# Kernel tuning notes

Measured on AMD Instinct MI355X. Metric: run time of the kernel, lower is better.

## Reference

```python
import jax, jax.numpy as jnp
import numpy as np

B, T, C, H, W = 2, 8, 256, 24, 24
NH = 8
HC = C // NH          # 32 head channels
KT, KHW = 3, 9        # offset conv kernel
ST, SHW = 2, 8        # offset conv stride
EPS = 1e-5


def _p(key, shape):
    return jax.random.normal(key, shape, dtype=jnp.float32) * 0.05


def setup_inputs() -> dict:
    ks = jax.random.split(jax.random.key(0), 16)
    return {
        "x": jax.random.normal(ks[0], (B, T, C, H, W), dtype=jnp.float32),
        "w_in": _p(ks[1], (C, C)), "b_in": _p(ks[2], (C,)),
        "w_q": _p(ks[3], (C, C)), "b_q": _p(ks[4], (C,)),
        "w_off_dw": _p(ks[5], (HC, 1, KT, KHW, KHW)), "b_off_dw": _p(ks[6], (HC,)),
        "ln_g": jnp.ones((HC,), jnp.float32), "ln_b": jnp.zeros((HC,), jnp.float32),
        "w_off_proj": _p(ks[7], (3, HC)),
        "w_k": _p(ks[8], (C, C)), "b_k": _p(ks[9], (C,)),
        "w_v": _p(ks[10], (C, C)), "b_v": _p(ks[11], (C,)),
        "rpe_w1": _p(ks[12], (32, 3)), "rpe_b1": _p(ks[13], (32,)),
        "rpe_w2": _p(ks[14], (1, 32)),
    }


def _conv1x1(x, w, b):
    # x: (B,C,T,H,W), w: (Co,Ci) -> pointwise Conv3d
    return jnp.einsum('bcthw,oc->bothw', x, w) + b[None, :, None, None, None]


def _trilinear(img, gx, gy, gz):
    # torch F.grid_sample(mode='bilinear', align_corners=True) for 5D input.
    # img: (G,Ch,T,H,W); gx->W axis, gy->H axis, gz->T axis, coords in [-1,1], shape (G,S)
    G, Ch, Td, Hd, Wd = img.shape
    ix = (gx + 1.0) * 0.5 * (Wd - 1)
    iy = (gy + 1.0) * 0.5 * (Hd - 1)
    iz = (gz + 1.0) * 0.5 * (Td - 1)
    x0 = jnp.floor(ix); y0 = jnp.floor(iy); z0 = jnp.floor(iz)
    fx = ix - x0; fy = iy - y0; fz = iz - z0
    x0i = jnp.clip(x0.astype(jnp.int32), 0, Wd - 1); x1i = jnp.clip(x0i + 1, 0, Wd - 1)
    y0i = jnp.clip(y0.astype(jnp.int32), 0, Hd - 1); y1i = jnp.clip(y0i + 1, 0, Hd - 1)
    z0i = jnp.clip(z0.astype(jnp.int32), 0, Td - 1); z1i = jnp.clip(z0i + 1, 0, Td - 1)
    bidx = jnp.arange(G)[:, None]

    def g(zi, yi, xi):
        return img[bidx, :, zi, yi, xi]  # (G,S,Ch)

    wz0, wz1 = (1.0 - fz)[..., None], fz[..., None]
    wy0, wy1 = (1.0 - fy)[..., None], fy[..., None]
    wx0, wx1 = (1.0 - fx)[..., None], fx[..., None]
    return (g(z0i, y0i, x0i) * wz0 * wy0 * wx0 + g(z0i, y0i, x1i) * wz0 * wy0 * wx1 +
            g(z0i, y1i, x0i) * wz0 * wy1 * wx0 + g(z0i, y1i, x1i) * wz0 * wy1 * wx1 +
            g(z1i, y0i, x0i) * wz1 * wy0 * wx0 + g(z1i, y0i, x1i) * wz1 * wy0 * wx1 +
            g(z1i, y1i, x0i) * wz1 * wy1 * wx0 + g(z1i, y1i, x1i) * wz1 * wy1 * wx1)


def reference(x, w_in, b_in, w_q, b_q, w_off_dw, b_off_dw, ln_g, ln_b, w_off_proj,
              w_k, b_k, w_v, b_v, rpe_w1, rpe_b1, rpe_w2):
    scale = HC ** (-0.5)
    xc = _conv1x1(jnp.transpose(x, (0, 2, 1, 3, 4)), w_in, b_in)       # (B,C,T,H,W)
    q = _conv1x1(xc, w_q, b_q)
    q_off = q.reshape(B * NH, HC, T, H, W)
    # depthwise offset conv: kernel (3,9,9), stride (2,8,8), pad (1,4,4)
    off = jax.lax.conv_general_dilated(
        q_off, w_off_dw, (ST, SHW, SHW),
        ((KT // 2, KT // 2), (KHW // 2, KHW // 2), (KHW // 2, KHW // 2)),
        dimension_numbers=('NCDHW', 'OIDHW', 'NCDHW'), feature_group_count=HC)
    off = off + b_off_dw[None, :, None, None, None]
    Tk, Hk, Wk = off.shape[2], off.shape[3], off.shape[4]
    o = jnp.transpose(off, (0, 2, 3, 4, 1))                             # (G,Tk,Hk,Wk,HC)
    mu = o.mean(-1, keepdims=True)
    var = ((o - mu) ** 2).mean(-1, keepdims=True)
    o = (o - mu) / jnp.sqrt(var + EPS) * ln_g + ln_b
    o = jax.nn.gelu(o, approximate=False)
    offset = jnp.einsum('bthwc,pc->bthwp', o, w_off_proj)               # (G,Tk,Hk,Wk,3)
    # reference points (linspace(0.5, K-0.5, K) normalized by (K-1))
    rt = ((jnp.arange(Tk, dtype=jnp.float32) + 0.5) / (Tk - 1.0)) * 2.0 - 1.0
    ry = ((jnp.arange(Hk, dtype=jnp.float32) + 0.5) / (Hk - 1.0)) * 2.0 - 1.0
    rx = ((jnp.arange(Wk, dtype=jnp.float32) + 0.5) / (Wk - 1.0)) * 2.0 - 1.0
    ref = jnp.stack(jnp.meshgrid(rt, ry, rx, indexing='ij'), axis=-1)   # (Tk,Hk,Wk,3)
    pos = jnp.clip(offset + ref, -1.0, 1.0)                             # offset_range_factor < 0 path
    G = B * NH
    n = Tk * Hk * Wk
    m = T * H * W
    posf = pos.reshape(G, n, 3)                                         # (t, y, x)
    # torch passes grid = pos[..., (0,2,1)] -> grid (x_w, y_h, z_t) = (pos_t, pos_x, pos_y)
    xs = _trilinear(xc.reshape(G, HC, T, H, W), posf[..., 0], posf[..., 2], posf[..., 1])  # (G,n,HC)
    x_sampled = jnp.transpose(xs, (0, 2, 1)).reshape(B, C, Tk, Hk, Wk)
    k = _conv1x1(x_sampled, w_k, b_k).reshape(G, HC, n)
    v = _conv1x1(x_sampled, w_v, b_v).reshape(G, HC, n)
    qf = q.reshape(G, HC, m)
    attn = jnp.einsum('bcm,bcn->bmn', qf, k) * scale                    # (G,m,n)
    # log-CPB bias (source normalizes y by W-1 and x by H-1; faithful)
    qt = (jnp.arange(T, dtype=jnp.float32) / (T - 1.0)) * 2.0 - 1.0
    qy = (jnp.arange(H, dtype=jnp.float32) / (W - 1.0)) * 2.0 - 1.0
    qx = (jnp.arange(W, dtype=jnp.float32) / (H - 1.0)) * 2.0 - 1.0
    qg = jnp.stack(jnp.meshgrid(qt, qy, qx, indexing='ij'), axis=-1).reshape(m, 3)
    disp = (qg[None, :, None, :] - posf[:, None, :, :]) * 4.0           # (G,m,n,3)
    disp = jnp.sign(disp) * jnp.log2(jnp.abs(disp) + 1.0) / 3.0         # log2(8) = 3
    hbias = jax.nn.relu(jnp.einsum('gmnp,hp->gmnh', disp, rpe_w1) + rpe_b1)
    attn = attn + jnp.einsum('gmnh,oh->gmno', hbias, rpe_w2)[..., 0]
    attn = jax.nn.softmax(attn, axis=2)
    out = jnp.einsum('bmn,bcn->bcm', attn, v).reshape(B, C, T, H, W)
    return jnp.transpose(out, (0, 2, 1, 3, 4))                          # (B,T,C,H,W)
```

## Files before the change

kernel.cpp:

```cpp
#include <hip/hip_runtime.h>
#include <hip/hip_bf16.h>

typedef unsigned short ushortT;
typedef __attribute__((ext_vector_type(8))) short bf16x8;
typedef __attribute__((ext_vector_type(4))) float f32x4;

#define WS_XC   0
#define WS_QB   2359296
#define WS_POS  3538944
#define WS_K    3540736
#define WS_V    3559168
#define WS_WC   3577600
#define WS_B512 3675904
#define WS_FLAG 3676416
#define WS_XHI  3677184
#define WS_XLO  4856832
#define WS_WHI  6036480
#define WS_WLO  6102016

__device__ __forceinline__ float bf2f(ushortT u) {
  union { unsigned int i; float f; } c; c.i = ((unsigned int)u) << 16; return c.f;
}
__device__ __forceinline__ ushortT f2bf(float f) {
  union { float f; unsigned int i; } c; c.f = f;
  unsigned int lsb = (c.i >> 16) & 1;
  return (ushortT)((c.i + 0x7fff + lsb) >> 16);
}
__device__ __forceinline__ float ldg_f(const void* p, int i, int bf) {
  return bf ? bf2f(((const ushortT*)p)[i]) : ((const float*)p)[i];
}

__global__ void k_detect(const void* x, int* flagout) {
  int lane = threadIdx.x;
  const ushortT* u = (const ushortT*)x;
  int wild = 0;
  for (int i = lane; i < 512; i += 64) {
    ushortT s = u[i];
    int e = (s >> 7) & 0xFF;
    if (e != 0 && (e < 90 || e > 160)) wild++;
  }
  for (int off = 32; off; off >>= 1) wild += __shfl_down(wild, off);
  if (lane == 0) flagout[0] = (wild > 40) ? 0 : 1;
}

__global__ __launch_bounds__(256) void k_wc(const void* w_in, const void* b_in, const void* w_q,
                                            const void* b_q, float* wc, float* bias512, const int* flag) {
  int o = blockIdx.x, tid = threadIdx.x, bf = flag[0];
  __shared__ float wq_s[256];
  __shared__ float red[256];
  wq_s[tid] = ldg_f(w_q, o * 256 + tid, bf);
  __syncthreads();
  float s = 0.f;
#pragma unroll 8
  for (int j = 0; j < 256; j++) s += wq_s[j] * ldg_f(w_in, j * 256 + tid, bf);
  wc[o * 256 + tid] = s;
  red[tid] = wq_s[tid] * ldg_f(b_in, tid, bf);
  __syncthreads();
  for (int m = 128; m; m >>= 1) {
    if (tid < m) red[tid] += red[tid + m];
    __syncthreads();
  }
  if (tid == 0) bias512[256 + o] = red[0] + ldg_f(b_q, o, bf);
  if (o == 0) bias512[tid] = ldg_f(b_in, tid, bf);
}

__global__ __launch_bounds__(256) void k_xsplit(const void* x, ushortT* xhi, ushortT* xlo,
                                                const int* flag) {
  int bf = flag[0];
  int i0 = (blockIdx.x * 256 + threadIdx.x) * 4;
  float v[4];
  if (bf) {
    ushort4 u = *(const ushort4*)((const ushortT*)x + i0);
    v[0] = bf2f(u.x); v[1] = bf2f(u.y); v[2] = bf2f(u.z); v[3] = bf2f(u.w);
  } else {
    float4 f = *(const float4*)((const float*)x + i0);
    v[0] = f.x; v[1] = f.y; v[2] = f.z; v[3] = f.w;
  }
  ushortT hi[4], lo[4];
#pragma unroll
  for (int j = 0; j < 4; j++) {
    hi[j] = f2bf(v[j]);
    lo[j] = f2bf(v[j] - bf2f(hi[j]));
  }
  *(ushort4*)(xhi + i0) = make_ushort4(hi[0], hi[1], hi[2], hi[3]);
  *(ushort4*)(xlo + i0) = make_ushort4(lo[0], lo[1], lo[2], lo[3]);
}

__global__ __launch_bounds__(256) void k_wsplit(const void* w_in, const float* wc,
                                                ushortT* whi, ushortT* wlo, const int* flag) {
  int o = blockIdx.x, k = threadIdx.x, bf = flag[0];
  float v = (o < 256) ? ldg_f(w_in, o * 256 + k, bf) : wc[(o - 256) * 256 + k];
  ushortT h = f2bf(v);
  whi[o * 256 + k] = h;
  wlo[o * 256 + k] = f2bf(v - bf2f(h));
}

__global__ __launch_bounds__(256) void k_gemm_mfma(const ushortT* xhi, const ushortT* xlo,
                                                   const ushortT* whi, const ushortT* wlo,
                                                   const float* bias512, float* xc, ushortT* qb) {
  __shared__ ushortT Ah[64 * 40], Al[64 * 40];
  __shared__ ushortT Bh[64 * 40], Bl[64 * 40];
  int tid = threadIdx.x;
  int bid = blockIdx.x;
  int colT = bid / 144, rowT = bid % 144;
  int col0 = colT * 64;
  int row0 = rowT * 64;
  int bt = row0 / 576;
  int hw0 = row0 % 576;
  const int isW = (col0 < 256);
  int ar = tid & 63, aoct = tid >> 6;
  int bn = tid >> 2, bko = tid & 3;
  const ushortT* bsrcH = whi + (col0 + bn) * 256;
  const ushortT* bsrcL = wlo + (col0 + bn) * 256;
  int w = tid >> 6, l = tid & 63;
  int wr = w >> 1, wcq = w & 1;
  int lr = l & 15, lk = l >> 4;
  f32x4 acc[2][2] = {};

  for (int kt = 0; kt < 8; kt++) {
    {
      int kbase = (bt * 256 + kt * 32 + aoct * 8) * 576 + hw0 + ar;
      unsigned int h[8], lo[8];
#pragma unroll
      for (int j = 0; j < 8; j++) {
        h[j]  = xhi[kbase + j * 576];
        lo[j] = xlo[kbase + j * 576];
      }
      int4 ph, pl;
      ph.x = (int)(h[0] | (h[1] << 16));   ph.y = (int)(h[2] | (h[3] << 16));
      ph.z = (int)(h[4] | (h[5] << 16));   ph.w = (int)(h[6] | (h[7] << 16));
      pl.x = (int)(lo[0] | (lo[1] << 16)); pl.y = (int)(lo[2] | (lo[3] << 16));
      pl.z = (int)(lo[4] | (lo[5] << 16)); pl.w = (int)(lo[6] | (lo[7] << 16));
      *(int4*)&Ah[ar * 40 + aoct * 8] = ph;
      *(int4*)&Al[ar * 40 + aoct * 8] = pl;
    }
    {
      int4 vh = *(const int4*)(bsrcH + kt * 32 + bko * 8);
      int4 vl = *(const int4*)(bsrcL + kt * 32 + bko * 8);
      *(int4*)&Bh[bn * 40 + bko * 8] = vh;
      *(int4*)&Bl[bn * 40 + bko * 8] = vl;
    }
    __syncthreads();
    bf16x8 a0h = *(const bf16x8*)&Ah[(wr * 32 + 0 * 16 + lr) * 40 + lk * 8];
    bf16x8 a1h = *(const bf16x8*)&Ah[(wr * 32 + 1 * 16 + lr) * 40 + lk * 8];
    bf16x8 a0l = *(const bf16x8*)&Al[(wr * 32 + 0 * 16 + lr) * 40 + lk * 8];
    bf16x8 a1l = *(const bf16x8*)&Al[(wr * 32 + 1 * 16 + lr) * 40 + lk * 8];
    bf16x8 b0h = *(const bf16x8*)&Bh[(wcq * 32 + 0 * 16 + lr) * 40 + lk * 8];
    bf16x8 b1h = *(const bf16x8*)&Bh[(wcq * 32 + 1 * 16 + lr) * 40 + lk * 8];
    bf16x8 b0l = *(const bf16x8*)&Bl[(wcq * 32 + 0 * 16 + lr) * 40 + lk * 8];
    bf16x8 b1l = *(const bf16x8*)&Bl[(wcq * 32 + 1 * 16 + lr) * 40 + lk * 8];
    acc[0][0] = __builtin_amdgcn_mfma_f32_16x16x32_bf16(a0h, b0h, acc[0][0], 0, 0, 0);
    acc[0][0] = __builtin_amdgcn_mfma_f32_16x16x32_bf16(a0h, b0l, acc[0][0], 0, 0, 0);
    acc[0][0] = __builtin_amdgcn_mfma_f32_16x16x32_bf16(a0l, b0h, acc[0][0], 0, 0, 0);
    acc[0][1] = __builtin_amdgcn_mfma_f32_16x16x32_bf16(a0h, b1h, acc[0][1], 0, 0, 0);
    acc[0][1] = __builtin_amdgcn_mfma_f32_16x16x32_bf16(a0h, b1l, acc[0][1], 0, 0, 0);
    acc[0][1] = __builtin_amdgcn_mfma_f32_16x16x32_bf16(a0l, b1h, acc[0][1], 0, 0, 0);
    acc[1][0] = __builtin_amdgcn_mfma_f32_16x16x32_bf16(a1h, b0h, acc[1][0], 0, 0, 0);
    acc[1][0] = __builtin_amdgcn_mfma_f32_16x16x32_bf16(a1h, b0l, acc[1][0], 0, 0, 0);
    acc[1][0] = __builtin_amdgcn_mfma_f32_16x16x32_bf16(a1l, b0h, acc[1][0], 0, 0, 0);
    acc[1][1] = __builtin_amdgcn_mfma_f32_16x16x32_bf16(a1h, b1h, acc[1][1], 0, 0, 0);
    acc[1][1] = __builtin_amdgcn_mfma_f32_16x16x32_bf16(a1h, b1l, acc[1][1], 0, 0, 0);
    acc[1][1] = __builtin_amdgcn_mfma_f32_16x16x32_bf16(a1l, b1h, acc[1][1], 0, 0, 0);
    __syncthreads();
  }
#pragma unroll
  for (int m = 0; m < 2; m++) {
#pragma unroll
    for (int n = 0; n < 2; n++) {
#pragma unroll
      for (int i = 0; i < 4; i++) {
        int row = row0 + wr * 32 + m * 16 + lk * 4 + i;
        int col = col0 + wcq * 32 + n * 16 + lr;
        float v = acc[m][n][i] + bias512[col];
        if (isW) xc[row * 256 + col] = v;
        else     qb[row * 256 + (col - 256)] = f2bf(v);
      }
    }
  }
}

__global__ __launch_bounds__(256) void k_offsets(const ushortT* qb, const void* w_dw, const void* b_dw,
                                                 const void* ln_g, const void* ln_b, const void* w_proj,
                                                 float* pos, const int* flag) {
  __shared__ float wdw[243 * 33];
  __shared__ float part[8][33];
  int bid = blockIdx.x;
  int g = bid / 36, nn = bid % 36;
  int b = g >> 3, nh = g & 7;
  int tk = nn / 9, hk = (nn / 3) % 3, wk = nn % 3;
  int tid = threadIdx.x;
  int ch = tid & 31, grp = tid >> 5;
  int bf = flag[0];
  for (int i = tid; i < 7776; i += 256) {
    int c = i / 243, tap = i % 243;
    wdw[tap * 33 + c] = ldg_f(w_dw, i, bf);
  }
  __syncthreads();
  float sum = 0.f;
  for (int tap = grp; tap < 243; tap += 8) {
    int dt = tap / 81, rem = tap % 81, dh = rem / 9, dw = rem % 9;
    int t = tk * 2 - 1 + dt, h = hk * 8 - 4 + dh, w = wk * 8 - 4 + dw;
    if (t < 0 || t >= 8 || h < 0 || h >= 24 || w < 0 || w >= 24) continue;
    float qv = bf2f(qb[((b * 8 + t) * 576 + h * 24 + w) * 256 + nh * 32 + ch]);
    sum += qv * wdw[tap * 33 + ch];
  }
  part[grp][ch] = sum;
  __syncthreads();
  if (tid < 32) {
    float v = ldg_f(b_dw, ch, bf);
#pragma unroll
    for (int j = 0; j < 8; j++) v += part[j][ch];
    float s1 = v;
    for (int m = 16; m; m >>= 1) s1 += __shfl_xor(s1, m);
    float mu = s1 * (1.f / 32.f);
    float d = v - mu;
    float s2 = d * d;
    for (int m = 16; m; m >>= 1) s2 += __shfl_xor(s2, m);
    float o = d * rsqrtf(s2 * (1.f / 32.f) + 1e-5f) * ldg_f(ln_g, ch, bf) + ldg_f(ln_b, ch, bf);
    o = 0.5f * o * (1.f + erff(o * 0.70710678118654752f));
    float res[3];
#pragma unroll
    for (int p = 0; p < 3; p++) {
      float t3 = o * ldg_f(w_proj, p * 32 + ch, bf);
      for (int m = 16; m; m >>= 1) t3 += __shfl_xor(t3, m);
      res[p] = t3;
    }
    if (ch == 0) {
      float ref0 = ((tk + 0.5f) / 3.f) * 2.f - 1.f;
      float ref1 = ((hk + 0.5f) / 2.f) * 2.f - 1.f;
      float ref2 = ((wk + 0.5f) / 2.f) * 2.f - 1.f;
      pos[bid * 3 + 0] = fminf(1.f, fmaxf(-1.f, res[0] + ref0));
      pos[bid * 3 + 1] = fminf(1.f, fmaxf(-1.f, res[1] + ref1));
      pos[bid * 3 + 2] = fminf(1.f, fmaxf(-1.f, res[2] + ref2));
    }
  }
}

__global__ __launch_bounds__(256) void k_svkv(const float* xc_rm, const float* pos,
                                              const void* w_k, const void* b_k,
                                              const void* w_v, const void* b_v,
                                              float* k_rm, float* v_rm, const int* flag) {
  int bx = blockIdx.x;
  int sel = bx & 1, row = bx >> 1;
  int b = row / 36, nn = row % 36;
  int tid = threadIdx.x;
  int bf = flag[0];
  __shared__ float a[256];
  {
    int nh = tid >> 5;
    int g = b * 8 + nh;
    float p0 = pos[(g * 36 + nn) * 3 + 0];
    float p1 = pos[(g * 36 + nn) * 3 + 1];
    float p2 = pos[(g * 36 + nn) * 3 + 2];
    float ix = (p0 + 1.f) * 0.5f * 23.f;
    float iy = (p2 + 1.f) * 0.5f * 23.f;
    float iz = (p1 + 1.f) * 0.5f * 7.f;
    float x0f = floorf(ix), y0f = floorf(iy), z0f = floorf(iz);
    float fx = ix - x0f, fy = iy - y0f, fz = iz - z0f;
    int x0 = min(max((int)x0f, 0), 23), x1 = min(x0 + 1, 23);
    int y0 = min(max((int)y0f, 0), 23), y1 = min(y0 + 1, 23);
    int z0 = min(max((int)z0f, 0), 7),  z1 = min(z0 + 1, 7);
#define AT(z, y, x) xc_rm[(((b * 8 + (z)) * 576 + (y) * 24 + (x)) * 256 + tid)]
    a[tid] =
      AT(z0, y0, x0) * (1.f - fz) * (1.f - fy) * (1.f - fx) + AT(z0, y0, x1) * (1.f - fz) * (1.f - fy) * fx +
      AT(z0, y1, x0) * (1.f - fz) * fy * (1.f - fx)         + AT(z0, y1, x1) * (1.f - fz) * fy * fx +
      AT(z1, y0, x0) * fz * (1.f - fy) * (1.f - fx)         + AT(z1, y0, x1) * fz * (1.f - fy) * fx +
      AT(z1, y1, x0) * fz * fy * (1.f - fx)                 + AT(z1, y1, x1) * fz * fy * fx;
#undef AT
  }
  __syncthreads();
  const void* w = sel ? w_v : w_k;
  const void* bb = sel ? b_v : b_k;
  float s = 0.f;
  if (bf) {
    const ushortT* wp = (const ushortT*)w + tid * 256;
#pragma unroll 4
    for (int c = 0; c < 256; c += 8) {
      ushort4 k0 = *(const ushort4*)(wp + c), k1 = *(const ushort4*)(wp + c + 4);
      s += a[c+0]*bf2f(k0.x) + a[c+1]*bf2f(k0.y) + a[c+2]*bf2f(k0.z) + a[c+3]*bf2f(k0.w)
         + a[c+4]*bf2f(k1.x) + a[c+5]*bf2f(k1.y) + a[c+6]*bf2f(k1.z) + a[c+7]*bf2f(k1.w);
    }
  } else {
    const float* wp = (const float*)w + tid * 256;
#pragma unroll 4
    for (int c = 0; c < 256; c += 4) {
      float4 k4 = *(const float4*)(wp + c);
      s += a[c]*k4.x + a[c+1]*k4.y + a[c+2]*k4.z + a[c+3]*k4.w;
    }
  }
  float* outp = sel ? v_rm : k_rm;
  outp[row * 256 + tid] = s + ldg_f(bb, tid, bf);
}

__global__ __launch_bounds__(256) void k_attn(const ushortT* qb, const float* k_rm, const float* v_rm,
                                              const float* pos, const void* rpe_w1, const void* rpe_b1,
                                              const void* rpe_w2, void* outp, const int* flag) {
  __shared__ float ks[36][32];
  __shared__ float vs[36][32];
  __shared__ float poss[36][4];
  __shared__ float4 wab[32];
  __shared__ float w2s[32];
  int g = blockIdx.y, b = g >> 3, nh = g & 7;
  int tid = threadIdx.x;
  int bf = flag[0];
  for (int e = tid; e < 36 * 32; e += 256) {
    int nn = e >> 5, ch = e & 31;
    ks[nn][ch] = k_rm[(b * 36 + nn) * 256 + nh * 32 + ch];
    vs[nn][ch] = v_rm[(b * 36 + nn) * 256 + nh * 32 + ch];
  }
  if (tid < 32) {
    wab[tid] = make_float4(ldg_f(rpe_w1, tid * 3 + 0, bf), ldg_f(rpe_w1, tid * 3 + 1, bf),
                           ldg_f(rpe_w1, tid * 3 + 2, bf), ldg_f(rpe_b1, tid, bf));
    w2s[tid] = ldg_f(rpe_w2, tid, bf);
  }
  if (tid < 108) poss[tid / 3][tid % 3] = pos[g * 108 + tid];
  __syncthreads();

  int mm = blockIdx.x * 256 + tid;
  int t = mm / 576, hw = mm % 576, hh = hw / 24, wwi = hw % 24;
  float qreg[32];
  const ushort4* qp = (const ushort4*)&qb[(b * 4608 + mm) * 256 + nh * 32];
#pragma unroll
  for (int i = 0; i < 8; i++) {
    ushort4 u = qp[i];
    qreg[i * 4 + 0] = bf2f(u.x); qreg[i * 4 + 1] = bf2f(u.y);
    qreg[i * 4 + 2] = bf2f(u.z); qreg[i * 4 + 3] = bf2f(u.w);
  }
  float qg0 = t * (2.f / 7.f) - 1.f;
  float qg1 = hh * (2.f / 23.f) - 1.f;
  float qg2 = wwi * (2.f / 23.f) - 1.f;
  const float scale = 0.17677669529663687f;
  float p[36];
  float mx = -1e30f;
#pragma unroll
  for (int nn = 0; nn < 36; nn++) {
    float s = 0.f;
#pragma unroll
    for (int ch = 0; ch < 32; ch++) s += qreg[ch] * ks[nn][ch];
    float d0 = (qg0 - poss[nn][0]) * 4.f;
    float d1 = (qg1 - poss[nn][1]) * 4.f;
    float d2 = (qg2 - poss[nn][2]) * 4.f;
    d0 = copysignf(__log2f(fabsf(d0) + 1.f) * (1.f / 3.f), d0);
    d1 = copysignf(__log2f(fabsf(d1) + 1.f) * (1.f / 3.f), d1);
    d2 = copysignf(__log2f(fabsf(d2) + 1.f) * (1.f / 3.f), d2);
    float bias = 0.f;
#pragma unroll
    for (int h = 0; h < 32; h++) {
      float4 w = wab[h];
      float hb = fmaf(d0, w.x, fmaf(d1, w.y, fmaf(d2, w.z, w.w)));
      bias = fmaf(fmaxf(hb, 0.f), w2s[h], bias);
    }
    float L = fmaf(s, scale, bias);
    p[nn] = L;
    mx = fmaxf(mx, L);
  }
  float se = 0.f;
#pragma unroll
  for (int nn = 0; nn < 36; nn++) {
    float e = __expf(p[nn] - mx);
    p[nn] = e;
    se += e;
  }
  float inv = 1.f / se;
  float acc[32] = {};
#pragma unroll
  for (int nn = 0; nn < 36; nn++) {
    float pr = p[nn] * inv;
#pragma unroll
    for (int ch = 0; ch < 32; ch++) acc[ch] += pr * vs[nn][ch];
  }
  int obase = ((b * 8 + t) * 256 + nh * 32) * 576 + hw;
  if (bf) {
    __hip_bfloat16* o = (__hip_bfloat16*)outp;
#pragma unroll
    for (int ch = 0; ch < 32; ch++) o[obase + ch * 576] = __float2bfloat16(acc[ch]);
  } else {
    float* o = (float*)outp;
#pragma unroll
    for (int ch = 0; ch < 32; ch++) o[obase + ch * 576] = acc[ch];
  }
}

extern "C" void kernel_launch(void* const* d_in, const int* in_sizes, int n_in,
                              void* d_out, int out_size, void* d_ws, size_t ws_size,
                              hipStream_t stream) {
  const void* x        = d_in[0];
  const void* w_in     = d_in[1];
  const void* b_in     = d_in[2];
  const void* w_q      = d_in[3];
  const void* b_q      = d_in[4];
  const void* w_off_dw = d_in[5];
  const void* b_off_dw = d_in[6];
  const void* ln_g     = d_in[7];
  const void* ln_b     = d_in[8];
  const void* w_off_pj = d_in[9];
  const void* w_k      = d_in[10];
  const void* b_k      = d_in[11];
  const void* w_v      = d_in[12];
  const void* b_v      = d_in[13];
  const void* rpe_w1   = d_in[14];
  const void* rpe_b1   = d_in[15];
  const void* rpe_w2   = d_in[16];

  float* ws    = (float*)d_ws;
  float* xc    = ws + WS_XC;
  ushortT* qb  = (ushortT*)(ws + WS_QB);
  float* pos   = ws + WS_POS;
  float* krm   = ws + WS_K;
  float* vrm   = ws + WS_V;
  float* wcf   = ws + WS_WC;
  float* b512  = ws + WS_B512;
  int* flag    = (int*)(ws + WS_FLAG);
  ushortT* xhi = (ushortT*)(ws + WS_XHI);
  ushortT* xlo = (ushortT*)(ws + WS_XLO);
  ushortT* whi = (ushortT*)(ws + WS_WHI);
  ushortT* wlo = (ushortT*)(ws + WS_WLO);

  k_detect<<<1, 64, 0, stream>>>(x, flag);
  k_wc<<<256, 256, 0, stream>>>(w_in, b_in, w_q, b_q, wcf, b512, flag);
  k_xsplit<<<2304, 256, 0, stream>>>(x, xhi, xlo, flag);
  k_wsplit<<<512, 256, 0, stream>>>(w_in, wcf, whi, wlo, flag);
  k_gemm_mfma<<<1152, 256, 0, stream>>>(xhi, xlo, whi, wlo, b512, xc, qb);
  k_offsets<<<576, 256, 0, stream>>>(qb, w_off_dw, b_off_dw, ln_g, ln_b, w_off_pj, pos, flag);
  k_svkv<<<144, 256, 0, stream>>>(xc, pos, w_k, b_k, w_v, b_v, krm, vrm, flag);
  k_attn<<<dim3(18, 16), 256, 0, stream>>>(qb, krm, vrm, pos, rpe_w1, rpe_b1, rpe_w2, d_out, flag);
}
```

Measured before the change: 125.1 us.

## Transpose x to row-major bf16 split and drop LDS staging in projection GEMM

The x hi/lo split kernel now transposes x through shared memory into a (token, channel) layout. This lets the MFMA GEMM load its A and B fragments straight from global memory with 16-byte vector loads, with no LDS staging and no barriers. The weight hi/lo split is folded into k_wc, which removes one kernel launch and the fp32 combined-weight buffer. In exchange, the GEMM depends on the cache for reuse across waves instead of shared memory, and the transpose adds a shared-memory pass.

```diff
diff --git a/kernel.cpp b/kernel.cpp
--- a/kernel.cpp
+++ b/kernel.cpp
@@ -10,7 +10,6 @@
 #define WS_POS  3538944
 #define WS_K    3540736
 #define WS_V    3559168
-#define WS_WC   3577600
 #define WS_B512 3675904
 #define WS_FLAG 3676416
 #define WS_XHI  3677184
@@ -44,7 +43,8 @@
 }
 
 __global__ __launch_bounds__(256) void k_wc(const void* w_in, const void* b_in, const void* w_q,
-                                            const void* b_q, float* wc, float* bias512, const int* flag) {
+                                            const void* b_q, ushortT* whi, ushortT* wlo,
+                                            float* bias512, const int* flag) {
   int o = blockIdx.x, tid = threadIdx.x, bf = flag[0];
   __shared__ float wq_s[256];
   __shared__ float red[256];
@@ -53,7 +53,13 @@
   float s = 0.f;
 #pragma unroll 8
   for (int j = 0; j < 256; j++) s += wq_s[j] * ldg_f(w_in, j * 256 + tid, bf);
-  wc[o * 256 + tid] = s;
+  ushortT h = f2bf(s);
+  whi[(256 + o) * 256 + tid] = h;
+  wlo[(256 + o) * 256 + tid] = f2bf(s - bf2f(h));
+  float w0 = ldg_f(w_in, o * 256 + tid, bf);
+  ushortT h0 = f2bf(w0);
+  whi[o * 256 + tid] = h0;
+  wlo[o * 256 + tid] = f2bf(w0 - bf2f(h0));
   red[tid] = wq_s[tid] * ldg_f(b_in, tid, bf);
   __syncthreads();
   for (int m = 128; m; m >>= 1) {
@@ -64,91 +70,66 @@
   if (o == 0) bias512[tid] = ldg_f(b_in, tid, bf);
 }
 
-__global__ __launch_bounds__(256) void k_xsplit(const void* x, ushortT* xhi, ushortT* xlo,
-                                                const int* flag) {
+__global__ __launch_bounds__(256) void k_xsplit_t(const void* x, ushortT* xhi, ushortT* xlo,
+                                                  const int* flag) {
+  __shared__ float tile[64][65];
+  int tid = threadIdx.x;
+  int bid = blockIdx.x;
+  int bt = bid / 36, rem = bid % 36;
+  int hwT = rem / 4, cT = rem % 4;
+  int hw0 = hwT * 64, c0 = cT * 64;
   int bf = flag[0];
-  int i0 = (blockIdx.x * 256 + threadIdx.x) * 4;
-  float v[4];
-  if (bf) {
-    ushort4 u = *(const ushort4*)((const ushortT*)x + i0);
-    v[0] = bf2f(u.x); v[1] = bf2f(u.y); v[2] = bf2f(u.z); v[3] = bf2f(u.w);
-  } else {
-    float4 f = *(const float4*)((const float*)x + i0);
-    v[0] = f.x; v[1] = f.y; v[2] = f.z; v[3] = f.w;
-  }
-  ushortT hi[4], lo[4];
-#pragma unroll
-  for (int j = 0; j < 4; j++) {
-    hi[j] = f2bf(v[j]);
-    lo[j] = f2bf(v[j] - bf2f(hi[j]));
-  }
-  *(ushort4*)(xhi + i0) = make_ushort4(hi[0], hi[1], hi[2], hi[3]);
-  *(ushort4*)(xlo + i0) = make_ushort4(lo[0], lo[1], lo[2], lo[3]);
-}
-
-__global__ __launch_bounds__(256) void k_wsplit(const void* w_in, const float* wc,
-                                                ushortT* whi, ushortT* wlo, const int* flag) {
-  int o = blockIdx.x, k = threadIdx.x, bf = flag[0];
-  float v = (o < 256) ? ldg_f(w_in, o * 256 + k, bf) : wc[(o - 256) * 256 + k];
-  ushortT h = f2bf(v);
-  whi[o * 256 + k] = h;
-  wlo[o * 256 + k] = f2bf(v - bf2f(h));
+  {
+    int lhw = tid & 63, cg = tid >> 6;
+#pragma unroll 4
+    for (int cc = 0; cc < 16; cc++) {
+      int cl = cg * 16 + cc;
+      tile[cl][lhw] = ldg_f(x, (bt * 256 + c0 + cl) * 576 + hw0 + lhw, bf);
+    }
+  }
+  __syncthreads();
+  {
+    int lc = tid & 63, hg = tid >> 6;
+#pragma unroll 4
+    for (int i = 0; i < 16; i++) {
+      int hl = hg + i * 4;
+      float v = tile[lc][hl];
+      ushortT h = f2bf(v);
+      int idx = (bt * 576 + hw0 + hl) * 256 + c0 + lc;
+      xhi[idx] = h;
+      xlo[idx] = f2bf(v - bf2f(h));
+    }
+  }
 }
 
 __global__ __launch_bounds__(256) void k_gemm_mfma(const ushortT* xhi, const ushortT* xlo,
                                                    const ushortT* whi, const ushortT* wlo,
                                                    const float* bias512, float* xc, ushortT* qb) {
-  __shared__ ushortT Ah[64 * 40], Al[64 * 40];
-  __shared__ ushortT Bh[64 * 40], Bl[64 * 40];
   int tid = threadIdx.x;
   int bid = blockIdx.x;
   int colT = bid / 144, rowT = bid % 144;
   int col0 = colT * 64;
   int row0 = rowT * 64;
-  int bt = row0 / 576;
-  int hw0 = row0 % 576;
   const int isW = (col0 < 256);
-  int ar = tid & 63, aoct = tid >> 6;
-  int bn = tid >> 2, bko = tid & 3;
-  const ushortT* bsrcH = whi + (col0 + bn) * 256;
-  const ushortT* bsrcL = wlo + (col0 + bn) * 256;
   int w = tid >> 6, l = tid & 63;
   int wr = w >> 1, wcq = w & 1;
   int lr = l & 15, lk = l >> 4;
+  const ushortT* paH = xhi + (row0 + wr * 32 + lr) * 256 + lk * 8;
+  const ushortT* paL = xlo + (row0 + wr * 32 + lr) * 256 + lk * 8;
+  const ushortT* pbH = whi + (col0 + wcq * 32 + lr) * 256 + lk * 8;
+  const ushortT* pbL = wlo + (col0 + wcq * 32 + lr) * 256 + lk * 8;
   f32x4 acc[2][2] = {};
-
+#pragma unroll
   for (int kt = 0; kt < 8; kt++) {
-    {
-      int kbase = (bt * 256 + kt * 32 + aoct * 8) * 576 + hw0 + ar;
-      unsigned int h[8], lo[8];
-#pragma unroll
-      for (int j = 0; j < 8; j++) {
-        h[j]  = xhi[kbase + j * 576];
-        lo[j] = xlo[kbase + j * 576];
-      }
-      int4 ph, pl;
-      ph.x = (int)(h[0] | (h[1] << 16));   ph.y = (int)(h[2] | (h[3] << 16));
-      ph.z = (int)(h[4] | (h[5] << 16));   ph.w = (int)(h[6] | (h[7] << 16));
-      pl.x = (int)(lo[0] | (lo[1] << 16)); pl.y = (int)(lo[2] | (lo[3] << 16));
-      pl.z = (int)(lo[4] | (lo[5] << 16)); pl.w = (int)(lo[6] | (lo[7] << 16));
-      *(int4*)&Ah[ar * 40 + aoct * 8] = ph;
-      *(int4*)&Al[ar * 40 + aoct * 8] = pl;
-    }
-    {
-      int4 vh = *(const int4*)(bsrcH + kt * 32 + bko * 8);
-      int4 vl = *(const int4*)(bsrcL + kt * 32 + bko * 8);
-      *(int4*)&Bh[bn * 40 + bko * 8] = vh;
-      *(int4*)&Bl[bn * 40 + bko * 8] = vl;
-    }
-    __syncthreads();
-    bf16x8 a0h = *(const bf16x8*)&Ah[(wr * 32 + 0 * 16 + lr) * 40 + lk * 8];
-    bf16x8 a1h = *(const bf16x8*)&Ah[(wr * 32 + 1 * 16 + lr) * 40 + lk * 8];
-    bf16x8 a0l = *(const bf16x8*)&Al[(wr * 32 + 0 * 16 + lr) * 40 + lk * 8];
-    bf16x8 a1l = *(const bf16x8*)&Al[(wr * 32 + 1 * 16 + lr) * 40 + lk * 8];
-    bf16x8 b0h = *(const bf16x8*)&Bh[(wcq * 32 + 0 * 16 + lr) * 40 + lk * 8];
-    bf16x8 b1h = *(const bf16x8*)&Bh[(wcq * 32 + 1 * 16 + lr) * 40 + lk * 8];
-    bf16x8 b0l = *(const bf16x8*)&Bl[(wcq * 32 + 0 * 16 + lr) * 40 + lk * 8];
-    bf16x8 b1l = *(const bf16x8*)&Bl[(wcq * 32 + 1 * 16 + lr) * 40 + lk * 8];
+    int ko = kt * 32;
+    bf16x8 a0h = *(const bf16x8*)(paH + ko);
+    bf16x8 a1h = *(const bf16x8*)(paH + 16 * 256 + ko);
+    bf16x8 a0l = *(const bf16x8*)(paL + ko);
+    bf16x8 a1l = *(const bf16x8*)(paL + 16 * 256 + ko);
+    bf16x8 b0h = *(const bf16x8*)(pbH + ko);
+    bf16x8 b1h = *(const bf16x8*)(pbH + 16 * 256 + ko);
+    bf16x8 b0l = *(const bf16x8*)(pbL + ko);
+    bf16x8 b1l = *(const bf16x8*)(pbL + 16 * 256 + ko);
     acc[0][0] = __builtin_amdgcn_mfma_f32_16x16x32_bf16(a0h, b0h, acc[0][0], 0, 0, 0);
     acc[0][0] = __builtin_amdgcn_mfma_f32_16x16x32_bf16(a0h, b0l, acc[0][0], 0, 0, 0);
     acc[0][0] = __builtin_amdgcn_mfma_f32_16x16x32_bf16(a0l, b0h, acc[0][0], 0, 0, 0);
@@ -161,7 +142,6 @@
     acc[1][1] = __builtin_amdgcn_mfma_f32_16x16x32_bf16(a1h, b1h, acc[1][1], 0, 0, 0);
     acc[1][1] = __builtin_amdgcn_mfma_f32_16x16x32_bf16(a1h, b1l, acc[1][1], 0, 0, 0);
     acc[1][1] = __builtin_amdgcn_mfma_f32_16x16x32_bf16(a1l, b1h, acc[1][1], 0, 0, 0);
-    __syncthreads();
   }
 #pragma unroll
   for (int m = 0; m < 2; m++) {
@@ -408,7 +388,6 @@
   float* pos   = ws + WS_POS;
   float* krm   = ws + WS_K;
   float* vrm   = ws + WS_V;
-  float* wcf   = ws + WS_WC;
   float* b512  = ws + WS_B512;
   int* flag    = (int*)(ws + WS_FLAG);
   ushortT* xhi = (ushortT*)(ws + WS_XHI);
@@ -417,9 +396,8 @@
   ushortT* wlo = (ushortT*)(ws + WS_WLO);
 
   k_detect<<<1, 64, 0, stream>>>(x, flag);
-  k_wc<<<256, 256, 0, stream>>>(w_in, b_in, w_q, b_q, wcf, b512, flag);
-  k_xsplit<<<2304, 256, 0, stream>>>(x, xhi, xlo, flag);
-  k_wsplit<<<512, 256, 0, stream>>>(w_in, wcf, whi, wlo, flag);
+  k_wc<<<256, 256, 0, stream>>>(w_in, b_in, w_q, b_q, whi, wlo, b512, flag);
+  k_xsplit_t<<<576, 256, 0, stream>>>(x, xhi, xlo, flag);
   k_gemm_mfma<<<1152, 256, 0, stream>>>(xhi, xlo, whi, wlo, b512, xc, qb);
   k_offsets<<<576, 256, 0, stream>>>(qb, w_off_dw, b_off_dw, ln_g, ln_b, w_off_pj, pos, flag);
   k_svkv<<<144, 256, 0, stream>>>(xc, pos, w_k, b_k, w_v, b_v, krm, vrm, flag);
```

Measured after the change: 146.7 us. 17.3% more time.
